# Kernel tuning notes

Hardware: AMD Instinct MI355X
Metric: run time of the kernel (lower is better)

The kernel has to match this reference:

```python
import jax, jax.numpy as jnp
import numpy as np

VOCAB = 32000
EMB = 1024
HID = 1024
CHUNK = 64
NCH = HID // CHUNK          # 16 master-gate chunks
G = 4 * HID + 2 * NCH       # 4128 gate width
T, B = 256, 64


def setup_inputs() -> dict:
    key = jax.random.key(0)
    ks = jax.random.split(key, 8)
    s = 0.02
    return {
        "tokens": jax.random.randint(ks[0], (T, B), 0, VOCAB),
        "emb": jax.random.normal(ks[1], (VOCAB, EMB), jnp.float32) * s,
        "W_ih0": jax.random.normal(ks[2], (EMB, G), jnp.float32) * s,
        "b_ih0": jnp.zeros((G,), jnp.float32),
        "W_hh0": jax.random.normal(ks[3], (HID, G), jnp.float32) * s,
        "b_hh0": jnp.zeros((G,), jnp.float32),
        "W_ih1": jax.random.normal(ks[4], (HID, G), jnp.float32) * s,
        "b_ih1": jnp.zeros((G,), jnp.float32),
        "W_hh1": jax.random.normal(ks[5], (HID, G), jnp.float32) * s,
        "b_hh1": jnp.zeros((G,), jnp.float32),
    }


def _cumsoftmax(x):
    # cumulative softmax along last dim (ordered-neuron master gate)
    return jnp.cumsum(jax.nn.softmax(x, axis=-1), axis=-1)


def _onlstm_layer(x, W_ih, b_ih, W_hh, b_hh):
    # x: (T, B, in_dim) -> (T, B, HID)
    t_in = jnp.einsum('tbi,ig->tbg', x, W_ih) + b_ih  # precomputed ih, as in torch code
    bsz = x.shape[1]
    h0 = jnp.zeros((bsz, HID), x.dtype)
    c0 = jnp.zeros((bsz, NCH, CHUNK), x.dtype)

    def step(carry, tin):
        hx, cx = carry
        gates = tin + hx @ W_hh + b_hh                      # (B, G)
        cingate = 1.0 - _cumsoftmax(gates[:, :NCH])         # (B, NCH)
        cforgetgate = _cumsoftmax(gates[:, NCH:2 * NCH])    # (B, NCH)
        rest = gates[:, 2 * NCH:].reshape(bsz, 4 * NCH, CHUNK)
        outgate, cell, ingate, forgetgate = jnp.split(rest, 4, axis=1)
        outgate = jax.nn.sigmoid(outgate)
        ingate = jax.nn.sigmoid(ingate)
        forgetgate = jax.nn.sigmoid(forgetgate)
        cell = jnp.tanh(cell)
        cing = cingate[:, :, None]
        cfg = cforgetgate[:, :, None]
        overlap = cfg * cing
        fgate = forgetgate * overlap + (cfg - overlap)
        igate = ingate * overlap + (cing - overlap)
        cy = fgate * cx + igate * cell                      # (B, NCH, CHUNK)
        hy = (outgate * jnp.tanh(cy)).reshape(bsz, HID)
        return (hy, cy), hy

    _, hs = jax.lax.scan(step, (h0, c0), t_in)
    return hs


def reference(tokens, emb, W_ih0, b_ih0, W_hh0, b_hh0, W_ih1, b_ih1, W_hh1, b_hh1):
    x = emb[tokens]                                         # (T, B, EMB)
    h1 = _onlstm_layer(x, W_ih0, b_ih0, W_hh0, b_hh0)
    h2 = _onlstm_layer(h1, W_ih1, b_ih1, W_hh1, b_hh1)
    mask = tokens != 0                                      # (T, B)
    return h2, mask
```

## Files before the change

### kernel.cpp

```cpp
#include <hip/hip_runtime.h>

typedef __attribute__((ext_vector_type(8))) short short8;
typedef __attribute__((ext_vector_type(4))) float f32x4;
typedef __attribute__((ext_vector_type(4))) int int4v;
typedef __attribute__((ext_vector_type(4))) unsigned short u16x4;
typedef unsigned short u16;

#define T_LEN 256
#define BATCH 64
#define HID   1024
#define GDIM  4128
#define K2    2048

__device__ __forceinline__ u16 f2bf(float f){
  unsigned u = __builtin_bit_cast(unsigned, f);
  return (u16)((u + 0x7fffu + ((u >> 16) & 1u)) >> 16);
}


__global__ __launch_bounds__(1024) void repackW(const float* __restrict__ Wih,
                                                const float* __restrict__ Whh,
                                                u16* __restrict__ Wt)
{
  __shared__ float tile[32][33];
  int k = blockIdx.x * 32 + threadIdx.y;
  int c = blockIdx.y * 32 + threadIdx.x;
  float v = (k < 1024) ? Wih[(size_t)k * GDIM + c]
                       : Whh[(size_t)(k - 1024) * GDIM + c];
  tile[threadIdx.y][threadIdx.x] = v;
  __syncthreads();
  int c2 = blockIdx.y * 32 + threadIdx.y;
  int k2 = blockIdx.x * 32 + threadIdx.x;
  Wt[(size_t)c2 * K2 + k2] = f2bf(tile[threadIdx.x][threadIdx.y]);
}

__global__ __launch_bounds__(256) void gatherX(const int* __restrict__ tokens,
                                               const float* __restrict__ emb,
                                               u16* __restrict__ x,
                                               float* __restrict__ maskout)
{
  int idx = blockIdx.x;
  int tok = tokens[idx];
  const f32x4* src = (const f32x4*)&emb[(size_t)tok * HID];
  f32x4 v = src[threadIdx.x];
  u16x4 o;
  #pragma unroll
  for (int j = 0; j < 4; ++j) o[j] = f2bf(v[j]);
  *(u16x4*)&x[(size_t)idx * HID + threadIdx.x * 4] = o;
  if (threadIdx.x == 0) maskout[idx] = (tok != 0) ? 1.0f : 0.0f;
}

__global__ __launch_bounds__(256) void biasK(const float* __restrict__ bih0, const float* __restrict__ bhh0,
                                             const float* __restrict__ bih1, const float* __restrict__ bhh1,
                                             float* __restrict__ bias0, float* __restrict__ bias1)
{
  int i = blockIdx.x * 256 + threadIdx.x;
  if (i < GDIM){ bias0[i] = bih0[i] + bhh0[i]; bias1[i] = bih1[i] + bhh1[i]; }
}

__global__ __launch_bounds__(256) void zeroK(int4v* __restrict__ p)
{
  int4v z = {0,0,0,0};
  p[blockIdx.x * 256 + threadIdx.x] = z;
}

__global__ __launch_bounds__(768) void stepA(
    const u16* __restrict__ Wt0, const u16* __restrict__ Wt1,
    const float* __restrict__ bias0, const float* __restrict__ bias1,
    const u16* __restrict__ x, const u16* __restrict__ h1,
    const u16* __restrict__ h2pp, const u16* __restrict__ zerob,
    float* __restrict__ gates0, float* __restrict__ gates1, int s)
{
  int w = blockIdx.x;
  int L = (w >= 86) ? 1 : 0;
  int wl = w - L * 86;
  int t = L ? (s - 1) : s;
  if (t < 0 || t >= T_LEN) return;
  int colbase = wl * 48;
  const u16* Wt = (L ? Wt1 : Wt0) + (size_t)colbase * K2;
  const float* bias = L ? bias1 : bias0;
  float* gates = L ? gates1 : gates0;
  const u16* p1 = L ? (h1 + (size_t)t * (BATCH * HID))
                    : (x  + (size_t)t * (BATCH * HID));
  const u16* p2;
  if (L) p2 = (t == 0) ? zerob : (h2pp + (size_t)((t - 1) & 1) * (BATCH * HID));
  else   p2 = (t == 0) ? zerob : (h1   + (size_t)(t - 1) * (BATCH * HID));

  __shared__ __align__(16) u16 Bs[48][1032];

  int tid  = threadIdx.x;
  int wave = tid >> 6, lane = tid & 63;
  int mtile = wave & 3, ntile = wave >> 2;
  int lo = lane & 15, hi = lane >> 4;
  int brow = mtile * 16 + lo;
  const u16* pa1 = p1 + (size_t)brow * HID;
  const u16* pa2 = p2 + (size_t)brow * HID;
  int bcol = ntile * 16 + lo;
  f32x4 acc = {0.f, 0.f, 0.f, 0.f};

  for (int ph = 0; ph < 2; ++ph) {
    __syncthreads();
    for (int i = tid; i < 48 * 128; i += 768) {
      int row = i >> 7;
      int off = (i & 127) << 3;
      *(int4v*)&Bs[row][off] =
          *(const int4v*)&Wt[(size_t)row * K2 + ph * 1024 + off];
    }
    __syncthreads();
    const u16* pa = ph ? pa2 : pa1;
    #pragma unroll 4
    for (int ks = 0; ks < 32; ++ks) {
      int k0 = ks * 32 + hi * 8;
      short8 a = *(const short8*)(pa + k0);
      short8 b = *(const short8*)&Bs[bcol][k0];
      acc = __builtin_amdgcn_mfma_f32_16x16x32_bf16(a, b, acc, 0, 0, 0);
    }
  }
  int colg = colbase + ntile * 16 + lo;
  float bv = bias[colg];
  #pragma unroll
  for (int j = 0; j < 4; ++j) {
    int br = mtile * 16 + hi * 4 + j;
    gates[(size_t)br * GDIM + colg] = acc[j] + bv;
  }
}

__global__ __launch_bounds__(256) void stepB(
    const float* __restrict__ gates0, const float* __restrict__ gates1,
    float* __restrict__ c0, float* __restrict__ c1,
    u16* __restrict__ h1, u16* __restrict__ h2pp,
    float* __restrict__ out, int s)
{
  int b = blockIdx.x, tid = threadIdx.x;
  __shared__ float sg[32];
  for (int L = 0; L < 2; ++L) {
    int t = L ? (s - 1) : s;
    if (t < 0 || t >= T_LEN) continue;
    __syncthreads();
    const float* g = (L ? gates1 : gates0) + (size_t)b * GDIM;
    if (tid < 32) sg[tid] = g[tid];
    __syncthreads();
    int e = tid * 4;
    int n = e >> 6;
    int k = e & 63;
    float m1 = -1e30f, m2 = -1e30f;
    #pragma unroll
    for (int i = 0; i < 16; ++i){ m1 = fmaxf(m1, sg[i]); m2 = fmaxf(m2, sg[16 + i]); }
    float s1 = 0.f, s2 = 0.f, cu1 = 0.f, cu2 = 0.f;
    #pragma unroll
    for (int i = 0; i < 16; ++i){
      float e1 = __expf(sg[i] - m1), e2 = __expf(sg[16 + i] - m2);
      s1 += e1; s2 += e2;
      if (i <= n){ cu1 += e1; cu2 += e2; }
    }
    float cin = 1.f - cu1 / s1;
    float cf  = cu2 / s2;
    float ov  = cf * cin;
    const float* gr = g + 32 + n * 64 + k;
    f32x4 og4 = *(const f32x4*)(gr);
    f32x4 ce4 = *(const f32x4*)(gr + 1024);
    f32x4 in4 = *(const f32x4*)(gr + 2048);
    f32x4 fg4 = *(const f32x4*)(gr + 3072);
    float* cbuf = (L ? c1 : c0) + (size_t)b * HID + e;
    f32x4 cx;
    if (t == 0) { cx = f32x4{0.f,0.f,0.f,0.f}; } else { cx = *(const f32x4*)cbuf; }
    f32x4 hy;
    #pragma unroll
    for (int j = 0; j < 4; ++j){
      float ogv = 1.f / (1.f + __expf(-og4[j]));
      float inv = 1.f / (1.f + __expf(-in4[j]));
      float fgv = 1.f / (1.f + __expf(-fg4[j]));
      float cev = tanhf(ce4[j]);
      float fga = fgv * ov + (cf - ov);
      float iga = inv * ov + (cin - ov);
      float cy  = fga * cx[j] + iga * cev;
      cx[j] = cy;
      hy[j] = ogv * tanhf(cy);
    }
    *(f32x4*)cbuf = cx;
    if (L == 0){
      u16x4 hb;
      #pragma unroll
      for (int j = 0; j < 4; ++j) hb[j] = f2bf(hy[j]);
      *(u16x4*)&h1[(size_t)t * (BATCH * HID) + b * HID + e] = hb;
    } else {
      *(f32x4*)&out[((size_t)t * BATCH + b) * HID + e] = hy;
      u16x4 hb;
      #pragma unroll
      for (int j = 0; j < 4; ++j) hb[j] = f2bf(hy[j]);
      *(u16x4*)&h2pp[(size_t)(t & 1) * (BATCH * HID) + b * HID + e] = hb;
    }
  }
}


extern "C" void kernel_launch(void* const* d_in, const int* in_sizes, int n_in,
                              void* d_out, int out_size, void* d_ws, size_t ws_size,
                              hipStream_t stream)
{
  (void)in_sizes; (void)n_in; (void)out_size; (void)ws_size;
  const int*   tokens = (const int*)d_in[0];
  const float* emb    = (const float*)d_in[1];
  const float* Wih0   = (const float*)d_in[2];
  const float* bih0   = (const float*)d_in[3];
  const float* Whh0   = (const float*)d_in[4];
  const float* bhh0   = (const float*)d_in[5];
  const float* Wih1   = (const float*)d_in[6];
  const float* bih1   = (const float*)d_in[7];
  const float* Whh1   = (const float*)d_in[8];
  const float* bhh1   = (const float*)d_in[9];
  float* out = (float*)d_out;

  char* ws = (char*)d_ws;
  u16*   Wt0    = (u16*)(ws);
  u16*   Wt1    = (u16*)(ws + 16908288);
  u16*   x      = (u16*)(ws + 33816576);
  u16*   h1     = (u16*)(ws + 67371008);
  float* bias0  = (float*)(ws + 100925440);
  float* bias1  = (float*)(ws + 100941952);
  float* gates0 = (float*)(ws + 100958464);
  float* gates1 = (float*)(ws + 102015232);
  float* c0     = (float*)(ws + 103072000);
  float* c1     = (float*)(ws + 103334144);
  u16*   zerob  = (u16*)(ws + 103596288);
  u16*   h2pp   = (u16*)(ws + 103727360);

  repackW<<<dim3(64,129), dim3(32,32), 0, stream>>>(Wih0, Whh0, Wt0);
  repackW<<<dim3(64,129), dim3(32,32), 0, stream>>>(Wih1, Whh1, Wt1);
  gatherX<<<16384, 256, 0, stream>>>(tokens, emb, x, out + 16777216);
  biasK<<<17, 256, 0, stream>>>(bih0, bhh0, bih1, bhh1, bias0, bias1);
  zeroK<<<96, 256, 0, stream>>>((int4v*)zerob);

  for (int s = 0; s <= 256; ++s){
    stepA<<<172, 768, 0, stream>>>(Wt0, Wt1, bias0, bias1, x, h1, h2pp, zerob,
                                   gates0, gates1, s);
    stepB<<<64, 256, 0, stream>>>(gates0, gates1, c0, c1, h1, h2pp, out, s);
  }
}
```

Baseline: 9.222 ms.

## Fuse per-step kernels into one persistent kernel with grid barriers

Replaces the 514 per-timestep launches of stepA/stepB with a single persistent kernel of 172 workgroups that loops over time and synchronises with an atomic-counter grid barrier. The pointwise update is done by 128 of those workgroups, covering both layers at once. This removes kernel launch overhead and inter-kernel gaps. In exchange it depends on all 172 workgroups being co-resident to avoid deadlock, and it adds two global barriers per step. Weights are still reloaded into LDS every step.

```diff
diff --git a/kernel.cpp b/kernel.cpp
--- a/kernel.cpp
+++ b/kernel.cpp
@@ -11,6 +11,7 @@
 #define HID   1024
 #define GDIM  4128
 #define K2    2048
+#define NWG   172
 
 __device__ __forceinline__ u16 f2bf(float f){
   unsigned u = __builtin_bit_cast(unsigned, f);
@@ -64,132 +65,147 @@
   p[blockIdx.x * 256 + threadIdx.x] = z;
 }
 
-__global__ __launch_bounds__(768) void stepA(
+__device__ __forceinline__ void gbar(unsigned* cnt, unsigned target){
+  __syncthreads();
+  if (threadIdx.x == 0){
+    __hip_atomic_fetch_add(cnt, 1u, __ATOMIC_ACQ_REL, __HIP_MEMORY_SCOPE_AGENT);
+    while (__hip_atomic_load(cnt, __ATOMIC_ACQUIRE, __HIP_MEMORY_SCOPE_AGENT) < target)
+      __builtin_amdgcn_s_sleep(2);
+  }
+  __syncthreads();
+}
+
+__global__ __launch_bounds__(768) void persist(
     const u16* __restrict__ Wt0, const u16* __restrict__ Wt1,
     const float* __restrict__ bias0, const float* __restrict__ bias1,
-    const u16* __restrict__ x, const u16* __restrict__ h1,
-    const u16* __restrict__ h2pp, const u16* __restrict__ zerob,
-    float* __restrict__ gates0, float* __restrict__ gates1, int s)
-{
-  int w = blockIdx.x;
-  int L = (w >= 86) ? 1 : 0;
-  int wl = w - L * 86;
-  int t = L ? (s - 1) : s;
-  if (t < 0 || t >= T_LEN) return;
+    const u16* __restrict__ x, u16* __restrict__ h1,
+    u16* __restrict__ h2pp, const u16* __restrict__ zerob,
+    float* __restrict__ gates0, float* __restrict__ gates1,
+    float* __restrict__ c0, float* __restrict__ c1,
+    float* __restrict__ out, unsigned* __restrict__ barCnt)
+{
+  __shared__ __align__(16) u16 Bs[48][1032];
+  __shared__ float sg[32];
+
+  int wg = blockIdx.x;
+  int tid = threadIdx.x;
+
+  int L = (wg >= 86) ? 1 : 0;
+  int wl = wg - L * 86;
   int colbase = wl * 48;
   const u16* Wt = (L ? Wt1 : Wt0) + (size_t)colbase * K2;
-  const float* bias = L ? bias1 : bias0;
-  float* gates = L ? gates1 : gates0;
-  const u16* p1 = L ? (h1 + (size_t)t * (BATCH * HID))
-                    : (x  + (size_t)t * (BATCH * HID));
-  const u16* p2;
-  if (L) p2 = (t == 0) ? zerob : (h2pp + (size_t)((t - 1) & 1) * (BATCH * HID));
-  else   p2 = (t == 0) ? zerob : (h1   + (size_t)(t - 1) * (BATCH * HID));
-
-  __shared__ __align__(16) u16 Bs[48][1032];
-
-  int tid  = threadIdx.x;
+  float* gatesA = L ? gates1 : gates0;
   int wave = tid >> 6, lane = tid & 63;
   int mtile = wave & 3, ntile = wave >> 2;
   int lo = lane & 15, hi = lane >> 4;
   int brow = mtile * 16 + lo;
-  const u16* pa1 = p1 + (size_t)brow * HID;
-  const u16* pa2 = p2 + (size_t)brow * HID;
   int bcol = ntile * 16 + lo;
-  f32x4 acc = {0.f, 0.f, 0.f, 0.f};
-
-  for (int ph = 0; ph < 2; ++ph) {
-    __syncthreads();
-    for (int i = tid; i < 48 * 128; i += 768) {
-      int row = i >> 7;
-      int off = (i & 127) << 3;
-      *(int4v*)&Bs[row][off] =
-          *(const int4v*)&Wt[(size_t)row * K2 + ph * 1024 + off];
+  int colg = colbase + ntile * 16 + lo;
+  float bv = (L ? bias1 : bias0)[colg];
+
+  int Lb = (wg >> 6) & 1, bb = wg & 63;
+  bool activeB = (wg < 128);
+
+  unsigned bidx = 0;
+  for (int s = 0; s <= T_LEN; ++s){
+    int t = L ? (s - 1) : s;
+    if (t >= 0 && t < T_LEN){
+      const u16* p1 = L ? (h1 + (size_t)t * (BATCH * HID))
+                        : (x  + (size_t)t * (BATCH * HID));
+      const u16* p2;
+      if (L) p2 = (t == 0) ? zerob : (h2pp + (size_t)((t - 1) & 1) * (BATCH * HID));
+      else   p2 = (t == 0) ? zerob : (h1   + (size_t)(t - 1) * (BATCH * HID));
+      const u16* pa1 = p1 + (size_t)brow * HID;
+      const u16* pa2 = p2 + (size_t)brow * HID;
+      f32x4 acc = {0.f, 0.f, 0.f, 0.f};
+      for (int ph = 0; ph < 2; ++ph){
+        __syncthreads();
+        for (int i = tid; i < 48 * 128; i += 768){
+          int row = i >> 7, off = (i & 127) << 3;
+          *(int4v*)&Bs[row][off] =
+              *(const int4v*)&Wt[(size_t)row * K2 + ph * 1024 + off];
+        }
+        __syncthreads();
+        const u16* pa = ph ? pa2 : pa1;
+        #pragma unroll 4
+        for (int ks = 0; ks < 32; ++ks){
+          int k0 = ks * 32 + hi * 8;
+          short8 a = *(const short8*)(pa + k0);
+          short8 b = *(const short8*)&Bs[bcol][k0];
+          acc = __builtin_amdgcn_mfma_f32_16x16x32_bf16(a, b, acc, 0, 0, 0);
+        }
+      }
+      #pragma unroll
+      for (int j = 0; j < 4; ++j){
+        int br = mtile * 16 + hi * 4 + j;
+        gatesA[(size_t)br * GDIM + colg] = acc[j] + bv;
+      }
     }
-    __syncthreads();
-    const u16* pa = ph ? pa2 : pa1;
-    #pragma unroll 4
-    for (int ks = 0; ks < 32; ++ks) {
-      int k0 = ks * 32 + hi * 8;
-      short8 a = *(const short8*)(pa + k0);
-      short8 b = *(const short8*)&Bs[bcol][k0];
-      acc = __builtin_amdgcn_mfma_f32_16x16x32_bf16(a, b, acc, 0, 0, 0);
+    ++bidx; gbar(barCnt, (unsigned)NWG * bidx);
+
+    {
+      int tb = Lb ? (s - 1) : s;
+      bool valid = activeB && (tb >= 0) && (tb < T_LEN);
+      const float* g = nullptr;
+      if (valid){
+        g = (Lb ? gates1 : gates0) + (size_t)bb * GDIM;
+        if (tid < 32) sg[tid] = g[tid];
+      }
+      __syncthreads();
+      if (valid && tid < 256){
+        int e = tid * 4;
+        int n = e >> 6;
+        int k = e & 63;
+        float m1 = -1e30f, m2 = -1e30f;
+        #pragma unroll
+        for (int i = 0; i < 16; ++i){ m1 = fmaxf(m1, sg[i]); m2 = fmaxf(m2, sg[16 + i]); }
+        float s1 = 0.f, s2 = 0.f, cu1 = 0.f, cu2 = 0.f;
+        #pragma unroll
+        for (int i = 0; i < 16; ++i){
+          float e1 = __expf(sg[i] - m1), e2 = __expf(sg[16 + i] - m2);
+          s1 += e1; s2 += e2;
+          if (i <= n){ cu1 += e1; cu2 += e2; }
+        }
+        float cin = 1.f - cu1 / s1;
+        float cf  = cu2 / s2;
+        float ov  = cf * cin;
+        const float* gr = g + 32 + n * 64 + k;
+        f32x4 og4 = *(const f32x4*)(gr);
+        f32x4 ce4 = *(const f32x4*)(gr + 1024);
+        f32x4 in4 = *(const f32x4*)(gr + 2048);
+        f32x4 fg4 = *(const f32x4*)(gr + 3072);
+        float* cbuf = (Lb ? c1 : c0) + (size_t)bb * HID + e;
+        f32x4 cx;
+        if (tb == 0) { cx = f32x4{0.f,0.f,0.f,0.f}; } else { cx = *(const f32x4*)cbuf; }
+        f32x4 hy;
+        #pragma unroll
+        for (int j = 0; j < 4; ++j){
+          float ogv = 1.f / (1.f + __expf(-og4[j]));
+          float inv = 1.f / (1.f + __expf(-in4[j]));
+          float fgv = 1.f / (1.f + __expf(-fg4[j]));
+          float cev = tanhf(ce4[j]);
+          float fga = fgv * ov + (cf - ov);
+          float iga = inv * ov + (cin - ov);
+          float cy  = fga * cx[j] + iga * cev;
+          cx[j] = cy;
+          hy[j] = ogv * tanhf(cy);
+        }
+        *(f32x4*)cbuf = cx;
+        if (Lb == 0){
+          u16x4 hb;
+          #pragma unroll
+          for (int j = 0; j < 4; ++j) hb[j] = f2bf(hy[j]);
+          *(u16x4*)&h1[(size_t)tb * (BATCH * HID) + bb * HID + e] = hb;
+        } else {
+          *(f32x4*)&out[((size_t)tb * BATCH + bb) * HID + e] = hy;
+          u16x4 hb;
+          #pragma unroll
+          for (int j = 0; j < 4; ++j) hb[j] = f2bf(hy[j]);
+          *(u16x4*)&h2pp[(size_t)(tb & 1) * (BATCH * HID) + bb * HID + e] = hb;
+        }
+      }
     }
-  }
-  int colg = colbase + ntile * 16 + lo;
-  float bv = bias[colg];
-  #pragma unroll
-  for (int j = 0; j < 4; ++j) {
-    int br = mtile * 16 + hi * 4 + j;
-    gates[(size_t)br * GDIM + colg] = acc[j] + bv;
-  }
-}
-
-__global__ __launch_bounds__(256) void stepB(
-    const float* __restrict__ gates0, const float* __restrict__ gates1,
-    float* __restrict__ c0, float* __restrict__ c1,
-    u16* __restrict__ h1, u16* __restrict__ h2pp,
-    float* __restrict__ out, int s)
-{
-  int b = blockIdx.x, tid = threadIdx.x;
-  __shared__ float sg[32];
-  for (int L = 0; L < 2; ++L) {
-    int t = L ? (s - 1) : s;
-    if (t < 0 || t >= T_LEN) continue;
-    __syncthreads();
-    const float* g = (L ? gates1 : gates0) + (size_t)b * GDIM;
-    if (tid < 32) sg[tid] = g[tid];
-    __syncthreads();
-    int e = tid * 4;
-    int n = e >> 6;
-    int k = e & 63;
-    float m1 = -1e30f, m2 = -1e30f;
-    #pragma unroll
-    for (int i = 0; i < 16; ++i){ m1 = fmaxf(m1, sg[i]); m2 = fmaxf(m2, sg[16 + i]); }
-    float s1 = 0.f, s2 = 0.f, cu1 = 0.f, cu2 = 0.f;
-    #pragma unroll
-    for (int i = 0; i < 16; ++i){
-      float e1 = __expf(sg[i] - m1), e2 = __expf(sg[16 + i] - m2);
-      s1 += e1; s2 += e2;
-      if (i <= n){ cu1 += e1; cu2 += e2; }
-    }
-    float cin = 1.f - cu1 / s1;
-    float cf  = cu2 / s2;
-    float ov  = cf * cin;
-    const float* gr = g + 32 + n * 64 + k;
-    f32x4 og4 = *(const f32x4*)(gr);
-    f32x4 ce4 = *(const f32x4*)(gr + 1024);
-    f32x4 in4 = *(const f32x4*)(gr + 2048);
-    f32x4 fg4 = *(const f32x4*)(gr + 3072);
-    float* cbuf = (L ? c1 : c0) + (size_t)b * HID + e;
-    f32x4 cx;
-    if (t == 0) { cx = f32x4{0.f,0.f,0.f,0.f}; } else { cx = *(const f32x4*)cbuf; }
-    f32x4 hy;
-    #pragma unroll
-    for (int j = 0; j < 4; ++j){
-      float ogv = 1.f / (1.f + __expf(-og4[j]));
-      float inv = 1.f / (1.f + __expf(-in4[j]));
-      float fgv = 1.f / (1.f + __expf(-fg4[j]));
-      float cev = tanhf(ce4[j]);
-      float fga = fgv * ov + (cf - ov);
-      float iga = inv * ov + (cin - ov);
-      float cy  = fga * cx[j] + iga * cev;
-      cx[j] = cy;
-      hy[j] = ogv * tanhf(cy);
-    }
-    *(f32x4*)cbuf = cx;
-    if (L == 0){
-      u16x4 hb;
-      #pragma unroll
-      for (int j = 0; j < 4; ++j) hb[j] = f2bf(hy[j]);
-      *(u16x4*)&h1[(size_t)t * (BATCH * HID) + b * HID + e] = hb;
-    } else {
-      *(f32x4*)&out[((size_t)t * BATCH + b) * HID + e] = hy;
-      u16x4 hb;
-      #pragma unroll
-      for (int j = 0; j < 4; ++j) hb[j] = f2bf(hy[j]);
-      *(u16x4*)&h2pp[(size_t)(t & 1) * (BATCH * HID) + b * HID + e] = hb;
-    }
+    ++bidx; gbar(barCnt, (unsigned)NWG * bidx);
   }
 }
 
@@ -224,16 +240,15 @@
   float* c1     = (float*)(ws + 103334144);
   u16*   zerob  = (u16*)(ws + 103596288);
   u16*   h2pp   = (u16*)(ws + 103727360);
+  unsigned* barCnt = (unsigned*)(ws + 103989504);
 
   repackW<<<dim3(64,129), dim3(32,32), 0, stream>>>(Wih0, Whh0, Wt0);
   repackW<<<dim3(64,129), dim3(32,32), 0, stream>>>(Wih1, Whh1, Wt1);
   gatherX<<<16384, 256, 0, stream>>>(tokens, emb, x, out + 16777216);
   biasK<<<17, 256, 0, stream>>>(bih0, bhh0, bih1, bhh1, bias0, bias1);
   zeroK<<<96, 256, 0, stream>>>((int4v*)zerob);
-
-  for (int s = 0; s <= 256; ++s){
-    stepA<<<172, 768, 0, stream>>>(Wt0, Wt1, bias0, bias1, x, h1, h2pp, zerob,
-                                   gates0, gates1, s);
-    stepB<<<64, 256, 0, stream>>>(gates0, gates1, c0, c1, h1, h2pp, out, s);
-  }
-}
+  hipMemsetAsync(barCnt, 0, 4, stream);
+
+  persist<<<NWG, 768, 0, stream>>>(Wt0, Wt1, bias0, bias1, x, h1, h2pp, zerob,
+                                   gates0, gates1, c0, c1, out, barCnt);
+}
```

New measurement: 14.27 ms. +54.7%, slower.
